# Kernel optimization log

Measured on AMD Instinct MI355X. Metric: run time of the kernel, lower is better.

## Reference

```python
import jax, jax.numpy as jnp
import numpy as np

N_CLUSTERS = 16
CLUSTER_SIZE = 32
N_HIDDEN = 16
N_FEATURES = N_CLUSTERS * CLUSTER_SIZE  # 512
BATCH = 131072


def setup_inputs() -> dict:
    key = jax.random.key(0)
    k_x, k_perm, k_ew, k_eb, k_dw, k_db = jax.random.split(key, 6)
    x = jax.random.normal(k_x, (BATCH, N_FEATURES), dtype=jnp.float32)
    # disjoint random feature clusters (a permutation split into groups)
    clusters = jax.random.permutation(k_perm, N_FEATURES).reshape(
        N_CLUSTERS, CLUSTER_SIZE).astype(jnp.int32)
    s_e = 1.0 / np.sqrt(CLUSTER_SIZE)
    s_d = 1.0 / np.sqrt(N_HIDDEN)
    enc_w = jax.random.uniform(k_ew, (N_CLUSTERS, N_HIDDEN, CLUSTER_SIZE),
                               minval=-s_e, maxval=s_e, dtype=jnp.float32)
    enc_b = jax.random.uniform(k_eb, (N_CLUSTERS, N_HIDDEN),
                               minval=-s_e, maxval=s_e, dtype=jnp.float32)
    dec_w = jax.random.uniform(k_dw, (N_CLUSTERS, CLUSTER_SIZE, N_HIDDEN),
                               minval=-s_d, maxval=s_d, dtype=jnp.float32)
    dec_b = jax.random.uniform(k_db, (N_CLUSTERS, CLUSTER_SIZE),
                               minval=-s_d, maxval=s_d, dtype=jnp.float32)
    return {"x": x, "clusters": clusters, "enc_w": enc_w, "enc_b": enc_b,
            "dec_w": dec_w, "dec_b": dec_b}


def reference(x, clusters, enc_w, enc_b, dec_w, dec_b):
    # gather per-cluster feature columns: [B, nC, cs]
    xi = x[:, clusters]
    # encoder: Linear(cs -> h) per cluster
    h = jnp.einsum('bnc,nhc->bnh', xi, enc_w) + enc_b  # [B, nC, h]
    # decoder: Linear(h -> cs) per cluster
    y = jnp.einsum('bnh,nch->bnc', h, dec_w) + dec_b   # [B, nC, cs]
    # concat cluster outputs along feature dim (cluster order)
    return y.reshape(x.shape[0], -1)  # [B, nC*cs]
```

## Files before the change

### kernel.cpp

```cpp
#include <hip/hip_runtime.h>


#define B_ROWS   131072
#define F        512
#define NC       16
#define CS       32
#define NH       16
#define NBLOCKS  1024
#define RPB      128
#define RPI      8
#define NITER    (RPB / RPI)

__global__ __launch_bounds__(256, 4)
void ensemble_kernel(const float* __restrict__ x,
                     const int*   __restrict__ clusters,
                     const float* __restrict__ enc_w,
                     const float* __restrict__ enc_b,
                     const float* __restrict__ dec_w,
                     const float* __restrict__ dec_b,
                     float*       __restrict__ out) {
    __shared__ float s_xi[RPI][F];
    __shared__ int   s_tgt[F];

    const int t = threadIdx.x;

    for (int j = t; j < F; j += 256) {
        int col = clusters[j];
        int nn = j >> 5, cc = j & 31;
        s_tgt[col] = (nn << 5) | ((cc + (nn << 2)) & 31);
    }
    __syncthreads();

    const int cbase = (t & 127) << 2;
    const int tgt0 = s_tgt[cbase + 0];
    const int tgt1 = s_tgt[cbase + 1];
    const int tgt2 = s_tgt[cbase + 2];
    const int tgt3 = s_tgt[cbase + 3];

    const int n  = t >> 4;
    const int c0 = (t & 15) << 1;

    float m0[32], m1[32];
    #pragma unroll
    for (int i = 0; i < 32; ++i) { m0[i] = 0.f; m1[i] = 0.f; }
    float b0 = dec_b[n * CS + c0];
    float b1 = dec_b[n * CS + c0 + 1];

    for (int h = 0; h < NH; ++h) {
        const float d0 = dec_w[(n * CS + c0)     * NH + h];
        const float d1 = dec_w[(n * CS + c0 + 1) * NH + h];
        const float eb = enc_b[n * NH + h];
        b0 += d0 * eb;
        b1 += d1 * eb;
        const float4* ew = (const float4*)(enc_w + (n * NH + h) * CS);
        #pragma unroll
        for (int k = 0; k < 8; ++k) {
            float4 e = ew[k];
            m0[4*k+0] += d0 * e.x;  m1[4*k+0] += d1 * e.x;
            m0[4*k+1] += d0 * e.y;  m1[4*k+1] += d1 * e.y;
            m0[4*k+2] += d0 * e.z;  m1[4*k+2] += d1 * e.z;
            m0[4*k+3] += d0 * e.w;  m1[4*k+3] += d1 * e.w;
        }
    }

    const int rhalf = t >> 7;
    const int row_block = blockIdx.x * RPB;
    const int xioff = n << 5;

    for (int it = 0; it < NITER; ++it) {
        const int r0 = row_block + it * RPI;

        float4 v[4];
        #pragma unroll
        for (int p = 0; p < 4; ++p) {
            const float* src = x + (size_t)(r0 + p * 2 + rhalf) * F + cbase;
            v[p] = *(const float4*)src;
        }

        __syncthreads();

        #pragma unroll
        for (int p = 0; p < 4; ++p) {
            float* dst = s_xi[p * 2 + rhalf];
            dst[tgt0] = v[p].x;
            dst[tgt1] = v[p].y;
            dst[tgt2] = v[p].z;
            dst[tgt3] = v[p].w;
        }

        __syncthreads();

        #pragma unroll
        for (int r = 0; r < RPI; ++r) {
            float a0 = b0, a1 = b1;
            const float* xr = &s_xi[r][xioff];
            #pragma unroll
            for (int k = 0; k < 8; ++k) {
                const int kk = (k + n) & 7;
                float4 xv = *(const float4*)(xr + (kk << 2));
                a0 += m0[4*k+0] * xv.x;  a1 += m1[4*k+0] * xv.x;
                a0 += m0[4*k+1] * xv.y;  a1 += m1[4*k+1] * xv.y;
                a0 += m0[4*k+2] * xv.z;  a1 += m1[4*k+2] * xv.z;
                a0 += m0[4*k+3] * xv.w;  a1 += m1[4*k+3] * xv.w;
            }
            float2 o = make_float2(a0, a1);
            *(float2*)(out + (size_t)(r0 + r) * F + xioff + c0) = o;
        }
    }
}

extern "C" void kernel_launch(void* const* d_in, const int* in_sizes, int n_in,
                              void* d_out, int out_size, void* d_ws, size_t ws_size,
                              hipStream_t stream) {
    const float* x      = (const float*)d_in[0];
    const int*   clus   = (const int*)  d_in[1];
    const float* enc_w  = (const float*)d_in[2];
    const float* enc_b  = (const float*)d_in[3];
    const float* dec_w  = (const float*)d_in[4];
    const float* dec_b  = (const float*)d_in[5];
    float*       out    = (float*)d_out;

    ensemble_kernel<<<NBLOCKS, 256, 0, stream>>>(x, clus, enc_w, enc_b, dec_w, dec_b, out);
}
```

Measured before the change: 476.2 us.

## Precompute fused weights in separate kernel and double-buffer shared input rows

Moves the per-cluster encoder-decoder weight product (M = dec_w·enc_w and the fused bias) into a small precompute kernel that writes to workspace, so each main block just loads its rows instead of recomputing them. The main kernel double-buffers the gathered x rows in shared memory, prefetching the next tile into registers while computing the current one, which drops one barrier per iteration. Each thread now produces four outputs per row with float4 stores instead of two, and the grid doubles to 2048 blocks of 64 rows with launch bounds lowered to 3. The cost is higher register pressure (128 weight registers per thread), double the shared memory, and an extra kernel launch.

```diff
diff --git a/kernel.cpp b/kernel.cpp
--- a/kernel.cpp
+++ b/kernel.cpp
@@ -1,25 +1,55 @@
 #include <hip/hip_runtime.h>
 
 
-#define B_ROWS   131072
 #define F        512
 #define NC       16
 #define CS       32
 #define NH       16
-#define NBLOCKS  1024
-#define RPB      128
+#define NBLOCKS  2048
+#define RPB      64
 #define RPI      8
 #define NITER    (RPB / RPI)
 
-__global__ __launch_bounds__(256, 4)
+__global__ void precompute_kernel(const float* __restrict__ enc_w,
+                                  const float* __restrict__ enc_b,
+                                  const float* __restrict__ dec_w,
+                                  const float* __restrict__ dec_b,
+                                  float* __restrict__ M,
+                                  float* __restrict__ bias) {
+    const int u = blockIdx.x * 256 + threadIdx.x;
+    if (u >= NC * CS) return;
+    const int n = u >> 5;
+
+    float m[32];
+    #pragma unroll
+    for (int i = 0; i < 32; ++i) m[i] = 0.f;
+    float b = dec_b[u];
+
+    for (int h = 0; h < NH; ++h) {
+        const float d = dec_w[u * NH + h];
+        b += d * enc_b[n * NH + h];
+        const float4* ew = (const float4*)(enc_w + (n * NH + h) * CS);
+        #pragma unroll
+        for (int k = 0; k < 8; ++k) {
+            float4 e = ew[k];
+            m[4*k+0] += d * e.x;  m[4*k+1] += d * e.y;
+            m[4*k+2] += d * e.z;  m[4*k+3] += d * e.w;
+        }
+    }
+    float4* Mo = (float4*)(M + u * CS);
+    #pragma unroll
+    for (int k = 0; k < 8; ++k)
+        Mo[k] = make_float4(m[4*k], m[4*k+1], m[4*k+2], m[4*k+3]);
+    bias[u] = b;
+}
+
+__global__ __launch_bounds__(256, 3)
 void ensemble_kernel(const float* __restrict__ x,
                      const int*   __restrict__ clusters,
-                     const float* __restrict__ enc_w,
-                     const float* __restrict__ enc_b,
-                     const float* __restrict__ dec_w,
-                     const float* __restrict__ dec_b,
+                     const float* __restrict__ M,
+                     const float* __restrict__ bias,
                      float*       __restrict__ out) {
-    __shared__ float s_xi[RPI][F];
+    __shared__ float s_xi[2][RPI][F];
     __shared__ int   s_tgt[F];
 
     const int t = threadIdx.x;
@@ -29,82 +59,88 @@
         int nn = j >> 5, cc = j & 31;
         s_tgt[col] = (nn << 5) | ((cc + (nn << 2)) & 31);
     }
+
+    const int rh    = t >> 7;
+    const int cbase = (t & 127) << 2;
+    const int n     = (t & 127) >> 3;
+    const int c0    = (t & 7) << 2;
+
+    float m[4][32];
+    #pragma unroll
+    for (int j = 0; j < 4; ++j) {
+        const float4* Mr = (const float4*)(M + (n * CS + c0 + j) * CS);
+        #pragma unroll
+        for (int k = 0; k < 8; ++k) {
+            float4 e = Mr[k];
+            m[j][4*k+0] = e.x;  m[j][4*k+1] = e.y;
+            m[j][4*k+2] = e.z;  m[j][4*k+3] = e.w;
+        }
+    }
+    const float4 bv = *(const float4*)(bias + n * CS + c0);
+
     __syncthreads();
 
-    const int cbase = (t & 127) << 2;
     const int tgt0 = s_tgt[cbase + 0];
     const int tgt1 = s_tgt[cbase + 1];
     const int tgt2 = s_tgt[cbase + 2];
     const int tgt3 = s_tgt[cbase + 3];
 
-    const int n  = t >> 4;
-    const int c0 = (t & 15) << 1;
+    const size_t row_block = (size_t)blockIdx.x * RPB;
+    const int xioff = n << 5;
 
-    float m0[32], m1[32];
+    float4 v[4];
     #pragma unroll
-    for (int i = 0; i < 32; ++i) { m0[i] = 0.f; m1[i] = 0.f; }
-    float b0 = dec_b[n * CS + c0];
-    float b1 = dec_b[n * CS + c0 + 1];
-
-    for (int h = 0; h < NH; ++h) {
-        const float d0 = dec_w[(n * CS + c0)     * NH + h];
-        const float d1 = dec_w[(n * CS + c0 + 1) * NH + h];
-        const float eb = enc_b[n * NH + h];
-        b0 += d0 * eb;
-        b1 += d1 * eb;
-        const float4* ew = (const float4*)(enc_w + (n * NH + h) * CS);
-        #pragma unroll
-        for (int k = 0; k < 8; ++k) {
-            float4 e = ew[k];
-            m0[4*k+0] += d0 * e.x;  m1[4*k+0] += d1 * e.x;
-            m0[4*k+1] += d0 * e.y;  m1[4*k+1] += d1 * e.y;
-            m0[4*k+2] += d0 * e.z;  m1[4*k+2] += d1 * e.z;
-            m0[4*k+3] += d0 * e.w;  m1[4*k+3] += d1 * e.w;
-        }
+    for (int p = 0; p < 4; ++p)
+        v[p] = *(const float4*)(x + (row_block + (size_t)(p * 2 + rh)) * F + cbase);
+    #pragma unroll
+    for (int p = 0; p < 4; ++p) {
+        float* dst = s_xi[0][p * 2 + rh];
+        dst[tgt0] = v[p].x;  dst[tgt1] = v[p].y;
+        dst[tgt2] = v[p].z;  dst[tgt3] = v[p].w;
     }
 
-    const int rhalf = t >> 7;
-    const int row_block = blockIdx.x * RPB;
-    const int xioff = n << 5;
+    for (int it = 0; it < NITER; ++it) {
+        const size_t r0 = row_block + (size_t)it * RPI;
 
-    for (int it = 0; it < NITER; ++it) {
-        const int r0 = row_block + it * RPI;
-
-        float4 v[4];
-        #pragma unroll
-        for (int p = 0; p < 4; ++p) {
-            const float* src = x + (size_t)(r0 + p * 2 + rhalf) * F + cbase;
-            v[p] = *(const float4*)src;
+        if (it + 1 < NITER) {
+            #pragma unroll
+            for (int p = 0; p < 4; ++p)
+                v[p] = *(const float4*)(x + (r0 + RPI + (size_t)(p * 2 + rh)) * F + cbase);
         }
 
         __syncthreads();
 
-        #pragma unroll
-        for (int p = 0; p < 4; ++p) {
-            float* dst = s_xi[p * 2 + rhalf];
-            dst[tgt0] = v[p].x;
-            dst[tgt1] = v[p].y;
-            dst[tgt2] = v[p].z;
-            dst[tgt3] = v[p].w;
-        }
-
-        __syncthreads();
+        const float (*buf)[F] = s_xi[it & 1];
 
         #pragma unroll
-        for (int r = 0; r < RPI; ++r) {
-            float a0 = b0, a1 = b1;
-            const float* xr = &s_xi[r][xioff];
+        for (int p2 = 0; p2 < 4; ++p2) {
+            const int r = p2 * 2 + rh;
+            const float* xr = &buf[r][xioff];
+            float a0 = bv.x, a1 = bv.y, a2 = bv.z, a3 = bv.w;
             #pragma unroll
             for (int k = 0; k < 8; ++k) {
                 const int kk = (k + n) & 7;
                 float4 xv = *(const float4*)(xr + (kk << 2));
-                a0 += m0[4*k+0] * xv.x;  a1 += m1[4*k+0] * xv.x;
-                a0 += m0[4*k+1] * xv.y;  a1 += m1[4*k+1] * xv.y;
-                a0 += m0[4*k+2] * xv.z;  a1 += m1[4*k+2] * xv.z;
-                a0 += m0[4*k+3] * xv.w;  a1 += m1[4*k+3] * xv.w;
+                a0 += m[0][4*k+0] * xv.x;  a1 += m[1][4*k+0] * xv.x;
+                a2 += m[2][4*k+0] * xv.x;  a3 += m[3][4*k+0] * xv.x;
+                a0 += m[0][4*k+1] * xv.y;  a1 += m[1][4*k+1] * xv.y;
+                a2 += m[2][4*k+1] * xv.y;  a3 += m[3][4*k+1] * xv.y;
+                a0 += m[0][4*k+2] * xv.z;  a1 += m[1][4*k+2] * xv.z;
+                a2 += m[2][4*k+2] * xv.z;  a3 += m[3][4*k+2] * xv.z;
+                a0 += m[0][4*k+3] * xv.w;  a1 += m[1][4*k+3] * xv.w;
+                a2 += m[2][4*k+3] * xv.w;  a3 += m[3][4*k+3] * xv.w;
             }
-            float2 o = make_float2(a0, a1);
-            *(float2*)(out + (size_t)(r0 + r) * F + xioff + c0) = o;
+            *(float4*)(out + (r0 + (size_t)r) * F + xioff + c0) =
+                make_float4(a0, a1, a2, a3);
+        }
+
+        if (it + 1 < NITER) {
+            #pragma unroll
+            for (int p = 0; p < 4; ++p) {
+                float* dst = s_xi[(it + 1) & 1][p * 2 + rh];
+                dst[tgt0] = v[p].x;  dst[tgt1] = v[p].y;
+                dst[tgt2] = v[p].z;  dst[tgt3] = v[p].w;
+            }
         }
     }
 }
@@ -120,5 +156,9 @@
     const float* dec_b  = (const float*)d_in[5];
     float*       out    = (float*)d_out;
 
-    ensemble_kernel<<<NBLOCKS, 256, 0, stream>>>(x, clus, enc_w, enc_b, dec_w, dec_b, out);
+    float* M    = (float*)d_ws;
+    float* bias = M + NC * CS * CS;
+
+    precompute_kernel<<<2, 256, 0, stream>>>(enc_w, enc_b, dec_w, dec_b, M, bias);
+    ensemble_kernel<<<NBLOCKS, 256, 0, stream>>>(x, clus, M, bias, out);
 }
```

New measurement: 801.0 us. 1.68x slower.
